# Performance work log

Hardware: AMD Instinct MI355X
Metric: run time of the kernel (lower is better)

## Reference

```python
import jax, jax.numpy as jnp
import numpy as np

M = 64            # multiplicity of 0e and of 1e irreps
NM = 2 * M        # num_mul = 128
SQ3 = float(np.sqrt(3.0))
SQ6 = float(np.sqrt(6.0))
C0 = float(np.sqrt(1.0 / 5.0))   # path weight for 0e outputs: sqrt(dim_out=1 / n_paths=5)
C1 = float(np.sqrt(3.0 / 5.0))   # path weight for 1e outputs: sqrt(dim_out=3 / n_paths=5)


def split_irreps(x):
    # x: [..., 256] -> scalars [..., 64], vectors [..., 64, 3]
    return x[:, :M], x[:, M:].reshape(x.shape[0], M, 3)


def merge_irreps(s, v):
    return jnp.concatenate([s, v.reshape(v.shape[0], -1)], axis=-1)


def o3_linear(x, W0, b0, W1):
    # e3nn o3.Linear: per-l mixing across multiplicities, shared over m, 1/sqrt(fan_in) norm, bias only on 0e
    s, v = split_irreps(x)
    s = s @ W0 / jnp.sqrt(jnp.float32(M)) + b0
    v = jnp.einsum('nuc,uv->nvc', v, W1) / jnp.sqrt(jnp.float32(M))
    return merge_irreps(s, v)


def ssp(x):
    return jax.nn.softplus(x) - jnp.log(2.0)


def norm_gate(x, W1, b1, W2, b2):
    # NormGate: gate 1e channels by MLP of [scalars, per-channel norms]
    s, v = split_irreps(x)
    nrm = jnp.sqrt(jnp.sum(v * v, axis=-1))             # [E, M]
    f0 = jnp.concatenate([s, nrm], axis=-1)             # [E, 2M]
    g = jax.nn.silu(f0 @ W1 + b1) @ W2 + b2             # [E, 2M]
    return merge_irreps(g[:, :M], v * g[:, M:, None])


def tp_node_pair(x, y, w):
    # weighted 'uuu' tensor product, instructions: (0e,0e->0e), (0e,1e->1e), (1e,0e->1e), (1e,1e->0e), (1e,1e->1e)
    xs, xv = split_irreps(x)
    ys, yv = split_irreps(y)
    w000, w011, w101, w110, w111 = jnp.split(w, 5, axis=-1)   # each [E, M]
    out_s = C0 * (w000 * xs * ys + w110 * jnp.sum(xv * yv, -1) / SQ3)
    out_v = C1 * (w011[..., None] * xs[..., None] * yv / SQ3
                  + w101[..., None] * xv * ys[..., None] / SQ3
                  + w111[..., None] * jnp.cross(xv, yv) / SQ6)
    return merge_irreps(out_s, out_v)


def reference(node_attr, edge_attr, node_pair_attr, Wi0, bi0, Wi1, gpW1, gpb1, gpW2, gpb2,
              Wn0, bn0, Wn1, feW1, feW2, fsW1, fsb1, fsW2, fsb2,
              gW1, gb1, gW2, gb2, Wo0, bo0, Wo1, edge_index):
    dst, src = edge_index[0], edge_index[1]
    # --- invariant branch: per-edge scalar descriptor s0 ---
    na0 = o3_linear(node_attr, Wi0, bi0, Wi1)
    s_d, v_d = split_irreps(na0[dst])
    s_s, v_s = split_irreps(na0[src])
    ip = jnp.sum(v_d * v_s, axis=-1) / 3.0               # InnerProduct of 1e channels (1/ir.dim)
    s0 = jnp.concatenate([s_d, s_s, ip], axis=-1)        # [E, 3M]
    # --- node feature branch ---
    h = norm_gate(node_attr, gpW1, gpb1, gpW2, gpb2)
    h = o3_linear(h, Wn0, bn0, Wn1)
    # --- edge-conditioned TP weights ---
    fe = ssp(edge_attr @ feW1 / jnp.sqrt(32.0)) @ feW2 / jnp.sqrt(8.0)   # FullyConnectedNet, [E, 5M]
    fs = jax.nn.silu(s0 @ fsW1 + fsb1) @ fsW2 + fsb2                     # [E, 5M]
    w = fe * fs
    # --- pair message ---
    pair = tp_node_pair(h[src], h[dst], w)
    pair = norm_gate(pair, gW1, gb1, gW2, gb2)
    pair = o3_linear(pair, Wo0, bo0, Wo1)
    return pair + node_pair_attr


def setup_inputs():
    key = jax.random.key(0)
    ks = jax.random.split(key, 20)
    N, E, EA, WN = 20000, 120000, 32, 320
    f32 = jnp.float32
    def nrm(k, shape, scale=1.0):
        return jax.random.normal(k, shape, dtype=f32) * scale
    return {
        'node_attr': nrm(ks[0], (N, 4 * M)),
        'edge_attr': nrm(ks[1], (E, EA)),
        'node_pair_attr': nrm(ks[2], (E, 4 * M)),
        'Wi0': nrm(ks[3], (M, M)), 'bi0': jnp.zeros((M,), f32), 'Wi1': nrm(ks[4], (M, M)),
        'gpW1': nrm(ks[5], (NM, NM), 1.0 / np.sqrt(NM)), 'gpb1': jnp.zeros((NM,), f32),
        'gpW2': nrm(ks[6], (NM, NM), 1.0 / np.sqrt(NM)), 'gpb2': jnp.zeros((NM,), f32),
        'Wn0': nrm(ks[7], (M, M)), 'bn0': jnp.zeros((M,), f32), 'Wn1': nrm(ks[8], (M, M)),
        'feW1': nrm(ks[9], (EA, 8)), 'feW2': nrm(ks[10], (8, WN)),
        'fsW1': nrm(ks[11], (3 * M, M), 1.0 / np.sqrt(3 * M)), 'fsb1': jnp.zeros((M,), f32),
        'fsW2': nrm(ks[12], (M, WN), 1.0 / np.sqrt(M)), 'fsb2': jnp.zeros((WN,), f32),
        'gW1': nrm(ks[13], (NM, NM), 1.0 / np.sqrt(NM)), 'gb1': jnp.zeros((NM,), f32),
        'gW2': nrm(ks[14], (NM, NM), 1.0 / np.sqrt(NM)), 'gb2': jnp.zeros((NM,), f32),
        'Wo0': nrm(ks[15], (M, M)), 'bo0': jnp.zeros((M,), f32), 'Wo1': nrm(ks[16], (M, M)),
        'edge_index': jax.random.randint(ks[17], (2, E), 0, N, dtype=jnp.int32),
    }
```

## Files before the change

### kernel.cpp

```cpp
#include <hip/hip_runtime.h>
#include <hip/hip_bf16.h>
#include <math.h>


static __device__ __forceinline__ float siluf(float x) { return x / (1.f + __expf(-x)); }
static __device__ __forceinline__ float sspf(float x) {
  return fmaxf(x, 0.f) + log1pf(__expf(-fabsf(x))) - 0.6931471805599453f;
}
static __device__ __forceinline__ short f2b(float x) {
  __hip_bfloat16 b = __float2bfloat16(x);
  short s; __builtin_memcpy(&s, &b, 2); return s;
}
static __device__ __forceinline__ float b2f(short s) {
  unsigned int u = ((unsigned int)(unsigned short)s) << 16;
  float f; __builtin_memcpy(&f, &u, 4); return f;
}

typedef __attribute__((ext_vector_type(4))) short short4v;
typedef __attribute__((ext_vector_type(8))) short short8v;
typedef __attribute__((ext_vector_type(16))) float f32x16;

static __device__ __forceinline__ short8v ld8(const short* p) {
  const short4v* q = (const short4v*)p;
  short4v a = q[0], b = q[1];
  short8v r;
  r[0] = a[0]; r[1] = a[1]; r[2] = a[2]; r[3] = a[3];
  r[4] = b[0]; r[5] = b[1]; r[6] = b[2]; r[7] = b[3];
  return r;
}

static __device__ __forceinline__ short8v gld8(const short* __restrict__ p) {
  return *reinterpret_cast<const short8v*>(p);
}

static __device__ __forceinline__ void sp2(short* hp, short* lp, float x) {
  short hh = f2b(x); *hp = hh; *lp = f2b(x - b2f(hh));
}

#define WOFF_FSW1 0
#define WOFF_FSW2 12288
#define WOFF_FEW1 32768
#define WOFF_FEW2 33792
#define WOFF_GW1  38912
#define WOFF_GW2  55296
#define WOFF_WO0  71680
#define WOFF_WO1  75776
#define NOFF_WI0  79872
#define NOFF_WI1  88064
#define NOFF_GP1  96256
#define NOFF_GP2  129024
#define NOFF_WN0  161792
#define NOFF_WN1  169984
#define W_ALL     178176

__global__ __launch_bounds__(256) void prep_weights(
    const float* __restrict__ fsW1, const float* __restrict__ fsW2,
    const float* __restrict__ feW1, const float* __restrict__ feW2,
    const float* __restrict__ gW1, const float* __restrict__ gW2,
    const float* __restrict__ Wo0, const float* __restrict__ Wo1,
    const float* __restrict__ Wi0, const float* __restrict__ Wi1,
    const float* __restrict__ gpW1, const float* __restrict__ gpW2,
    const float* __restrict__ Wn0, const float* __restrict__ Wn1,
    short* __restrict__ wsb)
{
  const int gt = blockIdx.x * blockDim.x + threadIdx.x;
  const int gs = gridDim.x * blockDim.x;
  for (int i = gt; i < 12288; i += gs) { int k = (i >> 10) * 16 + (i & 15), n = (i >> 4) & 63;  wsb[WOFF_FSW1 + i] = f2b(fsW1[k * 64 + n]); }
  for (int i = gt; i < 20480; i += gs) { int k = (i / 5120) * 16 + (i & 15), n = (i >> 4) % 320; wsb[WOFF_FSW2 + i] = f2b(fsW2[k * 320 + n]); }
  for (int i = gt; i < 1024; i += gs)  { int k = (i >> 9) * 16 + (i & 15),  n = (i >> 4) & 31;  wsb[WOFF_FEW1 + i] = (n < 8) ? f2b(feW1[k * 8 + n]) : 0; }
  for (int i = gt; i < 5120; i += gs)  { int k = i & 15,                    n = (i >> 4) % 320; wsb[WOFF_FEW2 + i] = (k < 8) ? f2b(feW2[k * 320 + n]) : 0; }
  for (int i = gt; i < 16384; i += gs) { int k = (i >> 11) * 16 + (i & 15), n = (i >> 4) & 127; wsb[WOFF_GW1 + i] = f2b(gW1[k * 128 + n]); }
  for (int i = gt; i < 16384; i += gs) { int k = (i >> 11) * 16 + (i & 15), n = (i >> 4) & 127; wsb[WOFF_GW2 + i] = f2b(gW2[k * 128 + n]); }
  for (int i = gt; i < 4096; i += gs)  { int k = (i >> 10) * 16 + (i & 15), n = (i >> 4) & 63;  wsb[WOFF_WO0 + i] = f2b(Wo0[k * 64 + n]); }
  for (int i = gt; i < 4096; i += gs)  { int k = (i >> 10) * 16 + (i & 15), n = (i >> 4) & 63;  wsb[WOFF_WO1 + i] = f2b(Wo1[k * 64 + n]); }
  for (int i = gt; i < 4096; i += gs)  { int k = (i >> 10) * 16 + (i & 15), n = (i >> 4) & 63;  float w = Wi0[k * 64 + n];  short hh = f2b(w); wsb[NOFF_WI0 + i] = hh; wsb[NOFF_WI0 + 4096 + i] = f2b(w - b2f(hh)); }
  for (int i = gt; i < 4096; i += gs)  { int k = (i >> 10) * 16 + (i & 15), n = (i >> 4) & 63;  float w = Wi1[k * 64 + n];  short hh = f2b(w); wsb[NOFF_WI1 + i] = hh; wsb[NOFF_WI1 + 4096 + i] = f2b(w - b2f(hh)); }
  for (int i = gt; i < 16384; i += gs) { int k = (i >> 11) * 16 + (i & 15), n = (i >> 4) & 127; float w = gpW1[k * 128 + n]; short hh = f2b(w); wsb[NOFF_GP1 + i] = hh; wsb[NOFF_GP1 + 16384 + i] = f2b(w - b2f(hh)); }
  for (int i = gt; i < 16384; i += gs) { int k = (i >> 11) * 16 + (i & 15), n = (i >> 4) & 127; float w = gpW2[k * 128 + n]; short hh = f2b(w); wsb[NOFF_GP2 + i] = hh; wsb[NOFF_GP2 + 16384 + i] = f2b(w - b2f(hh)); }
  for (int i = gt; i < 4096; i += gs)  { int k = (i >> 10) * 16 + (i & 15), n = (i >> 4) & 63;  float w = Wn0[k * 64 + n];  short hh = f2b(w); wsb[NOFF_WN0 + i] = hh; wsb[NOFF_WN0 + 4096 + i] = f2b(w - b2f(hh)); }
  for (int i = gt; i < 4096; i += gs)  { int k = (i >> 10) * 16 + (i & 15), n = (i >> 4) & 63;  float w = Wn1[k * 64 + n];  short hh = f2b(w); wsb[NOFF_WN1 + i] = hh; wsb[NOFF_WN1 + 4096 + i] = f2b(w - b2f(hh)); }
}

#define MFMA32(a, b, c) __builtin_amdgcn_mfma_f32_32x32x16_bf16(a, b, c, 0, 0, 0)

#define MFMA_HL(ah, al, bh, bl, acc) \
  do { acc = MFMA32((al), (bh), acc); acc = MFMA32((ah), (bl), acc); acc = MFMA32((ah), (bh), acc); } while (0)

#define XS_H 0
#define V0H  4352
#define F0H  17408
#define F0L  21632
#define TBH  0
#define TBL  4224
#define GVH  8704
#define GSH  21760
#define GSL  23936
#define NODE_LDS_SHORTS 26112

__global__ __launch_bounds__(256, 2) void node_kernel(
    const float* __restrict__ na,
    const float* __restrict__ bi0, const float* __restrict__ gpb1,
    const float* __restrict__ gpb2, const float* __restrict__ bn0,
    const short* __restrict__ wsb,
    float* __restrict__ na0, float* __restrict__ h, int N)
{
  __shared__ __align__(16) short smem[NODE_LDS_SHORTS];
  const int tid = threadIdx.x;
  const int wv = tid >> 6, ln = tid & 63;
  const int m32 = ln & 31, kh = ln >> 5;
  const int nb0 = blockIdx.x * 32;

  for (int i = 0; i < 8; ++i) {
    const int e = wv * 8 + i;
    int ng = nb0 + e; if (ng >= N) ng = N - 1;
    const float* xp = na + (size_t)ng * 256;
    const int u = ln;
    const float xs = xp[u];
    const float v0 = xp[64 + 3 * u], v1 = xp[64 + 3 * u + 1], v2 = xp[64 + 3 * u + 2];
    const float nr = sqrtf(v0 * v0 + v1 * v1 + v2 * v2);
    sp2(smem + XS_H + e * 68 + u,        smem + XS_H + 2176 + e * 68 + u, xs);
    sp2(smem + V0H + 0 * 4352 + e * 68 + u, smem + V0H + 0 * 4352 + 2176 + e * 68 + u, v0);
    sp2(smem + V0H + 1 * 4352 + e * 68 + u, smem + V0H + 1 * 4352 + 2176 + e * 68 + u, v1);
    sp2(smem + V0H + 2 * 4352 + e * 68 + u, smem + V0H + 2 * 4352 + 2176 + e * 68 + u, v2);
    sp2(smem + F0H + e * 132 + u,        smem + F0L + e * 132 + u, xs);
    sp2(smem + F0H + e * 132 + 64 + u,   smem + F0L + e * 132 + 64 + u, nr);
  }
  __syncthreads();

  {
    const int g = wv;
    const short* Ah = smem + (g == 0 ? XS_H : V0H + (g - 1) * 4352) + m32 * 68 + kh * 8;
    const short* Al = Ah + 2176;
    const int bofs = (g == 0) ? NOFF_WI0 : NOFF_WI1;
    for (int nt = 0; nt < 2; ++nt) {
      f32x16 acc = {};
      const int n = nt * 32 + m32;
      const short* Bh = wsb + bofs + n * 16 + kh * 8;
      const short* Bl = Bh + 4096;
#pragma unroll 2
      for (int k0 = 0; k0 < 4; ++k0) {
        short8v ah = ld8(Ah + k0 * 16), al = ld8(Al + k0 * 16);
        short8v bh = gld8(Bh + k0 * 1024), bl = gld8(Bl + k0 * 1024);
        MFMA_HL(ah, al, bh, bl, acc);
      }
      const float bias = (g == 0) ? bi0[n] : 0.f;
      const int off = (g == 0) ? n : 64 + 3 * n + (g - 1);
#pragma unroll
      for (int r = 0; r < 16; ++r) {
        int row = (r & 3) + 8 * (r >> 2) + 4 * kh;
        int ng = nb0 + row;
        if (ng < N) na0[(size_t)ng * 256 + off] = acc[r] * 0.125f + bias;
      }
    }
  }
  __syncthreads();

  {
    f32x16 acc = {};
    const int n = wv * 32 + m32;
    const short* Ah = smem + F0H + m32 * 132 + kh * 8;
    const short* Al = smem + F0L + m32 * 132 + kh * 8;
    const short* Bh = wsb + NOFF_GP1 + n * 16 + kh * 8;
    const short* Bl = Bh + 16384;
#pragma unroll 2
    for (int k0 = 0; k0 < 8; ++k0) {
      short8v ah = ld8(Ah + k0 * 16), al = ld8(Al + k0 * 16);
      short8v bh = gld8(Bh + k0 * 2048), bl = gld8(Bl + k0 * 2048);
      MFMA_HL(ah, al, bh, bl, acc);
    }
    const float bias = gpb1[n];
#pragma unroll
    for (int r = 0; r < 16; ++r) {
      int row = (r & 3) + 8 * (r >> 2) + 4 * kh;
      float t = siluf(acc[r] + bias);
      sp2(smem + TBH + row * 132 + n, smem + TBL + row * 132 + n, t);
    }
  }
  __syncthreads();

  {
    f32x16 acc = {};
    const int n = wv * 32 + m32;
    const short* Ah = smem + TBH + m32 * 132 + kh * 8;
    const short* Al = smem + TBL + m32 * 132 + kh * 8;
    const short* Bh = wsb + NOFF_GP2 + n * 16 + kh * 8;
    const short* Bl = Bh + 16384;
#pragma unroll 2
    for (int k0 = 0; k0 < 8; ++k0) {
      short8v ah = ld8(Ah + k0 * 16), al = ld8(Al + k0 * 16);
      short8v bh = gld8(Bh + k0 * 2048), bl = gld8(Bl + k0 * 2048);
      MFMA_HL(ah, al, bh, bl, acc);
    }
    const float bias = gpb2[n];
#pragma unroll
    for (int r = 0; r < 16; ++r) {
      int row = (r & 3) + 8 * (r >> 2) + 4 * kh;
      float val = acc[r] + bias;
      if (wv < 2) {
        sp2(smem + GSH + row * 68 + n, smem + GSL + row * 68 + n, val);
      } else {
        const int u = n - 64;
        int ng = nb0 + row; if (ng >= N) ng = N - 1;
        const float* vp = na + (size_t)ng * 256 + 64 + 3 * u;
#pragma unroll
        for (int c = 0; c < 3; ++c) {
          float pv = vp[c] * val;
          sp2(smem + GVH + c * 4352 + row * 68 + u,
              smem + GVH + c * 4352 + 2176 + row * 68 + u, pv);
        }
      }
    }
  }
  __syncthreads();

  {
    const int g = wv;
    const short* Ah = smem + (g == 0 ? GSH : GVH + (g - 1) * 4352) + m32 * 68 + kh * 8;
    const short* Al = Ah + 2176;
    const int bofs = (g == 0) ? NOFF_WN0 : NOFF_WN1;
    for (int nt = 0; nt < 2; ++nt) {
      f32x16 acc = {};
      const int n = nt * 32 + m32;
      const short* Bh = wsb + bofs + n * 16 + kh * 8;
      const short* Bl = Bh + 4096;
#pragma unroll 2
      for (int k0 = 0; k0 < 4; ++k0) {
        short8v ah = ld8(Ah + k0 * 16), al = ld8(Al + k0 * 16);
        short8v bh = gld8(Bh + k0 * 1024), bl = gld8(Bl + k0 * 1024);
        MFMA_HL(ah, al, bh, bl, acc);
      }
      const float bias = (g == 0) ? bn0[n] : 0.f;
      const int off = (g == 0) ? n : 64 + 3 * n + (g - 1);
#pragma unroll
      for (int r = 0; r < 16; ++r) {
        int row = (r & 3) + 8 * (r >> 2) + 4 * kh;
        int ng = nb0 + row;
        if (ng < N) h[(size_t)ng * 256 + off] = acc[r] * 0.125f + bias;
      }
    }
  }
}

#define A_HIDE  0
#define A_HID2  640
#define A_S0    2816
#define A_EA    9088
#define A_WB    2816
#define A_F0    13056
#define A_PV    17280
#define A_TB    2816
#define A_GATED 7040
#define ACT_TOTAL 23424
#define LDS_BYTES (ACT_TOTAL * 2)

__global__ __launch_bounds__(256, 3) void edge_kernel(
    const float* __restrict__ ea,
    const float* __restrict__ npa,
    const float* __restrict__ fsb1, const float* __restrict__ fsb2,
    const float* __restrict__ gb1, const float* __restrict__ gb2,
    const float* __restrict__ bo0,
    const int* __restrict__ eidx,
    const float* __restrict__ na0, const float* __restrict__ h,
    const short* __restrict__ wsb,
    float* __restrict__ out, int E)
{
  extern __shared__ __align__(16) short smem[];
  short* hidEb  = smem + A_HIDE;
  short* hid2b  = smem + A_HID2;
  short* s0b    = smem + A_S0;
  short* earowb = smem + A_EA;
  short* wb     = smem + A_WB;
  short* f0b    = smem + A_F0;
  short* pvb    = smem + A_PV;
  short* tb     = smem + A_TB;
  short* gated  = smem + A_GATED;

  const int tid = threadIdx.x;
  const int wv = tid >> 6, ln = tid & 63;
  const int m32 = ln & 31, kh = ln >> 5;
  const int e0 = blockIdx.x * 32;

  const float C0c = 0.4472135954999579f;
  const float C1c = 0.7745966692414834f;
  const float iS3 = 0.5773502691896258f;
  const float iS6 = 0.40824829046386307f;
  const float isq32 = 0.17677669529663687f;
  const float isq8 = 0.35355339059327373f;

  int dstI[8], srcI[8];
#pragma unroll
  for (int i = 0; i < 8; ++i) {
    int eg = e0 + wv * 8 + i; if (eg >= E) eg = E - 1;
    dstI[i] = eidx[eg]; srcI[i] = eidx[E + eg];
  }

  float hs_s[8], hd_s[8];
  float hs_v0[8], hs_v1[8], hs_v2[8], hd_v0[8], hd_v1[8], hd_v2[8];
#pragma unroll
  for (int i = 0; i < 8; ++i) {
    const float* hs = h + (size_t)srcI[i] * 256;
    const float* hd = h + (size_t)dstI[i] * 256;
    hs_s[i] = hs[ln];
    hd_s[i] = hd[ln];
    hs_v0[i] = hs[64 + 3 * ln];
    hs_v1[i] = hs[64 + 3 * ln + 1];
    hs_v2[i] = hs[64 + 3 * ln + 2];
    hd_v0[i] = hd[64 + 3 * ln];
    hd_v1[i] = hd[64 + 3 * ln + 1];
    hd_v2[i] = hd[64 + 3 * ln + 2];
  }

  for (int i = tid; i < 32 * 32; i += 256) {
    int e = i >> 5, k = i & 31;
    int eg = e0 + e; if (eg >= E) eg = E - 1;
    earowb[e * 36 + k] = f2b(ea[(size_t)eg * 32 + k]);
  }
  for (int i = tid; i < 640; i += 256) hidEb[i] = 0;
#pragma unroll
  for (int i = 0; i < 8; ++i) {
    const int e = wv * 8 + i;
    const float* nd = na0 + (size_t)dstI[i] * 256;
    const float* ns = na0 + (size_t)srcI[i] * 256;
    const int u = ln;
    float ip = nd[64 + 3 * u] * ns[64 + 3 * u] + nd[64 + 3 * u + 1] * ns[64 + 3 * u + 1]
             + nd[64 + 3 * u + 2] * ns[64 + 3 * u + 2];
    s0b[e * 196 + u] = f2b(nd[u]);
    s0b[e * 196 + 64 + u] = f2b(ns[u]);
    s0b[e * 196 + 128 + u] = f2b(ip * (1.f / 3.f));
  }
  __syncthreads();

  if (wv < 2) {
    f32x16 acc = {};
    const int n = wv * 32 + m32;
    const short* A = s0b + m32 * 196 + kh * 8;
    const short* B = wsb + WOFF_FSW1 + n * 16 + kh * 8;
#pragma unroll
    for (int k0 = 0; k0 < 12; ++k0)
      acc = MFMA32(ld8(A + k0 * 16), gld8(B + k0 * 1024), acc);
    const float bias = fsb1[n];
#pragma unroll
    for (int r = 0; r < 16; ++r) {
      int row = (r & 3) + 8 * (r >> 2) + 4 * kh;
      hid2b[row * 68 + n] = f2b(siluf(acc[r] + bias));
    }
  } else if (wv == 2) {
    f32x16 acc = {};
    const short* A = earowb + m32 * 36 + kh * 8;
    const short* B = wsb + WOFF_FEW1 + m32 * 16 + kh * 8;
#pragma unroll
    for (int k0 = 0; k0 < 2; ++k0)
      acc = MFMA32(ld8(A + k0 * 16), gld8(B + k0 * 512), acc);
    if (m32 < 8) {
#pragma unroll
      for (int r = 0; r < 16; ++r) {
        int row = (r & 3) + 8 * (r >> 2) + 4 * kh;
        hidEb[row * 20 + m32] = f2b(sspf(acc[r] * isq32));
      }
    }
  }
  __syncthreads();

  for (int nt = wv; nt < 10; nt += 4) {
    const int n = nt * 32 + m32;
    f32x16 aF = {};
    aF = MFMA32(ld8(hidEb + m32 * 20 + kh * 8), gld8(wsb + WOFF_FEW2 + n * 16 + kh * 8), aF);
    f32x16 aS = {};
    const short* A = hid2b + m32 * 68 + kh * 8;
    const short* B = wsb + WOFF_FSW2 + n * 16 + kh * 8;
#pragma unroll
    for (int k0 = 0; k0 < 4; ++k0)
      aS = MFMA32(ld8(A + k0 * 16), gld8(B + k0 * 5120), aS);
    const float bias = fsb2[n];
#pragma unroll
    for (int r = 0; r < 16; ++r) {
      int row = (r & 3) + 8 * (r >> 2) + 4 * kh;
      wb[row * 320 + n] = f2b((aS[r] + bias) * (aF[r] * isq8));
    }
  }
  __syncthreads();

#pragma unroll
  for (int i = 0; i < 8; ++i) {
    const int e = wv * 8 + i;
    const int u = ln;
    const float w0 = b2f(wb[e * 320 + u]);
    const float w1 = b2f(wb[e * 320 + u + 64]);
    const float w2 = b2f(wb[e * 320 + u + 128]);
    const float w3 = b2f(wb[e * 320 + u + 192]);
    const float w4 = b2f(wb[e * 320 + u + 256]);
    const float xs = hs_s[i], ys = hd_s[i];
    const float xv0 = hs_v0[i], xv1 = hs_v1[i], xv2 = hs_v2[i];
    const float yv0 = hd_v0[i], yv1 = hd_v1[i], yv2 = hd_v2[i];
    const float ipv = xv0 * yv0 + xv1 * yv1 + xv2 * yv2;
    const float cr0 = xv1 * yv2 - xv2 * yv1;
    const float cr1 = xv2 * yv0 - xv0 * yv2;
    const float cr2 = xv0 * yv1 - xv1 * yv0;
    const float ps = C0c * (w0 * xs * ys + w3 * ipv * iS3);
    const float k011 = C1c * iS3 * w1 * xs;
    const float k101 = C1c * iS3 * w2 * ys;
    const float k111 = C1c * iS6 * w4;
    const float pv0 = k011 * yv0 + k101 * xv0 + k111 * cr0;
    const float pv1 = k011 * yv1 + k101 * xv1 + k111 * cr1;
    const float pv2 = k011 * yv2 + k101 * xv2 + k111 * cr2;
    f0b[e * 132 + u] = f2b(ps);
    f0b[e * 132 + 64 + u] = f2b(sqrtf(pv0 * pv0 + pv1 * pv1 + pv2 * pv2));
    pvb[e * 192 + 3 * u + 0] = f2b(pv0);
    pvb[e * 192 + 3 * u + 1] = f2b(pv1);
    pvb[e * 192 + 3 * u + 2] = f2b(pv2);
  }
  __syncthreads();

  {
    f32x16 acc = {};
    const int n = wv * 32 + m32;
    const short* A = f0b + m32 * 132 + kh * 8;
    const short* B = wsb + WOFF_GW1 + n * 16 + kh * 8;
#pragma unroll
    for (int k0 = 0; k0 < 8; ++k0)
      acc = MFMA32(ld8(A + k0 * 16), gld8(B + k0 * 2048), acc);
    const float bias = gb1[n];
#pragma unroll
    for (int r = 0; r < 16; ++r) {
      int row = (r & 3) + 8 * (r >> 2) + 4 * kh;
      tb[row * 132 + n] = f2b(siluf(acc[r] + bias));
    }
  }
  __syncthreads();

  float npv[2][16];
  {
#pragma unroll
    for (int nt = 0; nt < 2; ++nt) {
      const int n = nt * 32 + m32;
      const int off = (wv == 0) ? n : 64 + 3 * n + (wv - 1);
#pragma unroll
      for (int r = 0; r < 16; ++r) {
        int row = (r & 3) + 8 * (r >> 2) + 4 * kh;
        int eg = e0 + row;
        npv[nt][r] = (eg < E) ? npa[(size_t)eg * 256 + off] : 0.f;
      }
    }
  }
  {
    f32x16 acc = {};
    const int n = wv * 32 + m32;
    const short* A = tb + m32 * 132 + kh * 8;
    const short* B = wsb + WOFF_GW2 + n * 16 + kh * 8;
#pragma unroll
    for (int k0 = 0; k0 < 8; ++k0)
      acc = MFMA32(ld8(A + k0 * 16), gld8(B + k0 * 2048), acc);
    const float bias = gb2[n];
#pragma unroll
    for (int r = 0; r < 16; ++r) {
      int row = (r & 3) + 8 * (r >> 2) + 4 * kh;
      float val = acc[r] + bias;
      if (wv < 2) {
        gated[row * 68 + n] = f2b(val);
      } else {
        int u = n - 64;
        float p0 = b2f(pvb[row * 192 + 3 * u + 0]);
        float p1 = b2f(pvb[row * 192 + 3 * u + 1]);
        float p2 = b2f(pvb[row * 192 + 3 * u + 2]);
        gated[2176 * 1 + row * 68 + u] = f2b(p0 * val);
        gated[2176 * 2 + row * 68 + u] = f2b(p1 * val);
        gated[2176 * 3 + row * 68 + u] = f2b(p2 * val);
      }
    }
  }
  __syncthreads();

  {
    const short* A = gated + 2176 * wv + m32 * 68 + kh * 8;
    const int bofs = (wv == 0) ? WOFF_WO0 : WOFF_WO1;
#pragma unroll
    for (int nt = 0; nt < 2; ++nt) {
      f32x16 acc = {};
      const int n = nt * 32 + m32;
      const short* B = wsb + bofs + n * 16 + kh * 8;
#pragma unroll
      for (int k0 = 0; k0 < 4; ++k0)
        acc = MFMA32(ld8(A + k0 * 16), gld8(B + k0 * 1024), acc);
      const float bias = (wv == 0) ? bo0[n] : 0.f;
      const int off = (wv == 0) ? n : 64 + 3 * n + (wv - 1);
#pragma unroll
      for (int r = 0; r < 16; ++r) {
        int row = (r & 3) + 8 * (r >> 2) + 4 * kh;
        int eg = e0 + row;
        if (eg < E)
          out[(size_t)eg * 256 + off] = acc[r] * 0.125f + bias + npv[nt][r];
      }
    }
  }
}

extern "C" void kernel_launch(void* const* d_in, const int* in_sizes, int n_in,
                              void* d_out, int out_size, void* d_ws, size_t ws_size,
                              hipStream_t stream) {
  const float* node_attr = (const float*)d_in[0];
  const float* edge_attr = (const float*)d_in[1];
  const float* npa  = (const float*)d_in[2];
  const float* Wi0  = (const float*)d_in[3];
  const float* bi0  = (const float*)d_in[4];
  const float* Wi1  = (const float*)d_in[5];
  const float* gpW1 = (const float*)d_in[6];
  const float* gpb1 = (const float*)d_in[7];
  const float* gpW2 = (const float*)d_in[8];
  const float* gpb2 = (const float*)d_in[9];
  const float* Wn0  = (const float*)d_in[10];
  const float* bn0  = (const float*)d_in[11];
  const float* Wn1  = (const float*)d_in[12];
  const float* feW1 = (const float*)d_in[13];
  const float* feW2 = (const float*)d_in[14];
  const float* fsW1 = (const float*)d_in[15];
  const float* fsb1 = (const float*)d_in[16];
  const float* fsW2 = (const float*)d_in[17];
  const float* fsb2 = (const float*)d_in[18];
  const float* gW1  = (const float*)d_in[19];
  const float* gb1  = (const float*)d_in[20];
  const float* gW2  = (const float*)d_in[21];
  const float* gb2  = (const float*)d_in[22];
  const float* Wo0  = (const float*)d_in[23];
  const float* bo0  = (const float*)d_in[24];
  const float* Wo1  = (const float*)d_in[25];
  const int* eidx = (const int*)d_in[26];

  const int N = in_sizes[0] / 256;
  const int E = in_sizes[1] / 32;

  float* na0 = (float*)d_ws;
  float* h = na0 + (size_t)N * 256;
  short* wsb = (short*)(h + (size_t)N * 256);

  (void)hipFuncSetAttribute((const void*)edge_kernel,
                            hipFuncAttributeMaxDynamicSharedMemorySize,
                            LDS_BYTES);

  prep_weights<<<96, 256, 0, stream>>>(fsW1, fsW2, feW1, feW2, gW1, gW2, Wo0, Wo1,
                                       Wi0, Wi1, gpW1, gpW2, Wn0, Wn1, wsb);
  node_kernel<<<(N + 31) / 32, 256, 0, stream>>>(node_attr, bi0, gpb1, gpb2, bn0,
                                                 wsb, na0, h, N);
  edge_kernel<<<(E + 31) / 32, 256, LDS_BYTES, stream>>>(
      edge_attr, npa, fsb1, fsb2, gb1, gb2, bo0, eidx, na0, h, wsb, (float*)d_out, E);
}
```

Before: 437.8 us.

## Consolidate edge-kernel LDS into one reused buffer and fuse gating into final GEMM

```diff
diff --git a/kernel.cpp b/kernel.cpp
--- a/kernel.cpp
+++ b/kernel.cpp
@@ -241,19 +241,16 @@
   }
 }
 
-#define A_HIDE  0
-#define A_HID2  640
-#define A_S0    2816
-#define A_EA    9088
-#define A_WB    2816
-#define A_F0    13056
-#define A_PV    17280
-#define A_TB    2816
-#define A_GATED 7040
-#define ACT_TOTAL 23424
-#define LDS_BYTES (ACT_TOTAL * 2)
-
-__global__ __launch_bounds__(256, 3) void edge_kernel(
+#define EU_STRIDE 324
+#define A_S0   0
+#define A_EA   6272
+#define A_HIDE 10368
+#define A_HID2 11008
+#define A_TB   13184
+#define EDGE_LDS_SHORTS 17408
+#define LDS_BYTES (EDGE_LDS_SHORTS * 2)
+
+__global__ __launch_bounds__(256, 4) void edge_kernel(
     const float* __restrict__ ea,
     const float* __restrict__ npa,
     const float* __restrict__ fsb1, const float* __restrict__ fsb2,
@@ -265,15 +262,12 @@
     float* __restrict__ out, int E)
 {
   extern __shared__ __align__(16) short smem[];
+  short* U      = smem;
+  short* s0b    = smem + A_S0;
+  short* earowb = smem + A_EA;
   short* hidEb  = smem + A_HIDE;
   short* hid2b  = smem + A_HID2;
-  short* s0b    = smem + A_S0;
-  short* earowb = smem + A_EA;
-  short* wb     = smem + A_WB;
-  short* f0b    = smem + A_F0;
-  short* pvb    = smem + A_PV;
   short* tb     = smem + A_TB;
-  short* gated  = smem + A_GATED;
 
   const int tid = threadIdx.x;
   const int wv = tid >> 6, ln = tid & 63;
@@ -375,7 +369,7 @@
 #pragma unroll
     for (int r = 0; r < 16; ++r) {
       int row = (r & 3) + 8 * (r >> 2) + 4 * kh;
-      wb[row * 320 + n] = f2b((aS[r] + bias) * (aF[r] * isq8));
+      U[row * EU_STRIDE + n] = f2b((aS[r] + bias) * (aF[r] * isq8));
     }
   }
   __syncthreads();
@@ -384,11 +378,12 @@
   for (int i = 0; i < 8; ++i) {
     const int e = wv * 8 + i;
     const int u = ln;
-    const float w0 = b2f(wb[e * 320 + u]);
-    const float w1 = b2f(wb[e * 320 + u + 64]);
-    const float w2 = b2f(wb[e * 320 + u + 128]);
-    const float w3 = b2f(wb[e * 320 + u + 192]);
-    const float w4 = b2f(wb[e * 320 + u + 256]);
+    short* row = U + e * EU_STRIDE;
+    const float w0 = b2f(row[u]);
+    const float w1 = b2f(row[u + 64]);
+    const float w2 = b2f(row[u + 128]);
+    const float w3 = b2f(row[u + 192]);
+    const float w4 = b2f(row[u + 256]);
     const float xs = hs_s[i], ys = hd_s[i];
     const float xv0 = hs_v0[i], xv1 = hs_v1[i], xv2 = hs_v2[i];
     const float yv0 = hd_v0[i], yv1 = hd_v1[i], yv2 = hd_v2[i];
@@ -403,18 +398,18 @@
     const float pv0 = k011 * yv0 + k101 * xv0 + k111 * cr0;
     const float pv1 = k011 * yv1 + k101 * xv1 + k111 * cr1;
     const float pv2 = k011 * yv2 + k101 * xv2 + k111 * cr2;
-    f0b[e * 132 + u] = f2b(ps);
-    f0b[e * 132 + 64 + u] = f2b(sqrtf(pv0 * pv0 + pv1 * pv1 + pv2 * pv2));
-    pvb[e * 192 + 3 * u + 0] = f2b(pv0);
-    pvb[e * 192 + 3 * u + 1] = f2b(pv1);
-    pvb[e * 192 + 3 * u + 2] = f2b(pv2);
+    row[u] = f2b(ps);
+    row[64 + u] = f2b(sqrtf(pv0 * pv0 + pv1 * pv1 + pv2 * pv2));
+    row[132 + u] = f2b(pv0);
+    row[132 + 64 + u] = f2b(pv1);
+    row[132 + 128 + u] = f2b(pv2);
   }
   __syncthreads();
 
   {
     f32x16 acc = {};
     const int n = wv * 32 + m32;
-    const short* A = f0b + m32 * 132 + kh * 8;
+    const short* A = U + m32 * EU_STRIDE + kh * 8;
     const short* B = wsb + WOFF_GW1 + n * 16 + kh * 8;
 #pragma unroll
     for (int k0 = 0; k0 < 8; ++k0)
@@ -454,35 +449,35 @@
 #pragma unroll
     for (int r = 0; r < 16; ++r) {
       int row = (r & 3) + 8 * (r >> 2) + 4 * kh;
-      float val = acc[r] + bias;
-      if (wv < 2) {
-        gated[row * 68 + n] = f2b(val);
-      } else {
-        int u = n - 64;
-        float p0 = b2f(pvb[row * 192 + 3 * u + 0]);
-        float p1 = b2f(pvb[row * 192 + 3 * u + 1]);
-        float p2 = b2f(pvb[row * 192 + 3 * u + 2]);
-        gated[2176 * 1 + row * 68 + u] = f2b(p0 * val);
-        gated[2176 * 2 + row * 68 + u] = f2b(p1 * val);
-        gated[2176 * 3 + row * 68 + u] = f2b(p2 * val);
-      }
-    }
-  }
-  __syncthreads();
-
-  {
-    const short* A = gated + 2176 * wv + m32 * 68 + kh * 8;
+      U[row * EU_STRIDE + n] = f2b(acc[r] + bias);
+    }
+  }
+  __syncthreads();
+
+  {
+    const int c = wv - 1;
     const int bofs = (wv == 0) ? WOFF_WO0 : WOFF_WO1;
+    const short* rowp = U + m32 * EU_STRIDE;
 #pragma unroll
     for (int nt = 0; nt < 2; ++nt) {
       f32x16 acc = {};
       const int n = nt * 32 + m32;
       const short* B = wsb + bofs + n * 16 + kh * 8;
 #pragma unroll
-      for (int k0 = 0; k0 < 4; ++k0)
-        acc = MFMA32(ld8(A + k0 * 16), gld8(B + k0 * 1024), acc);
+      for (int k0 = 0; k0 < 4; ++k0) {
+        short8v a;
+        if (wv == 0) {
+          a = ld8(rowp + kh * 8 + k0 * 16);
+        } else {
+          short8v pvf = ld8(rowp + 132 + c * 64 + kh * 8 + k0 * 16);
+          short8v gvf = ld8(rowp + 64 + kh * 8 + k0 * 16);
+#pragma unroll
+          for (int j = 0; j < 8; ++j) a[j] = f2b(b2f(pvf[j]) * b2f(gvf[j]));
+        }
+        acc = MFMA32(a, gld8(B + k0 * 1024), acc);
+      }
       const float bias = (wv == 0) ? bo0[n] : 0.f;
-      const int off = (wv == 0) ? n : 64 + 3 * n + (wv - 1);
+      const int off = (wv == 0) ? n : 64 + 3 * n + c;
 #pragma unroll
       for (int r = 0; r < 16; ++r) {
         int row = (r & 3) + 8 * (r >> 2) + 4 * kh;
```

After: 447.4 us. +2.2%, slower.
